# Kernel tuning notes

Hardware: AMD Instinct MI355X
Metric: run time of the kernel (lower is better)

The kernel has to match this reference:

```python
import jax, jax.numpy as jnp
import numpy as np

B, S, H, N = 2, 2048, 1024, 16
HN = H // N  # head dim = 64
EPS = 1e-12


def setup_inputs() -> dict:
    key = jax.random.key(0)
    ks = jax.random.split(key, 8)
    scale = 0.02
    return {
        "hidden_states": jax.random.normal(ks[0], (B, S, H), dtype=jnp.float32),
        "attention_mask": jnp.zeros((B, 1, 1, S), dtype=jnp.float32),
        "W_qkv": jax.random.normal(ks[1], (3 * H, H), dtype=jnp.float32) * scale,
        "b_qkv": jnp.zeros((3 * H,), dtype=jnp.float32),
        "W_out": jax.random.normal(ks[2], (H, H), dtype=jnp.float32) * scale,
        "b_out": jnp.zeros((H,), dtype=jnp.float32),
        "ln_gamma": jnp.ones((H,), dtype=jnp.float32),
        "ln_beta": jnp.zeros((H,), dtype=jnp.float32),
    }


def reference(hidden_states, attention_mask, W_qkv, b_qkv, W_out, b_out, ln_gamma, ln_beta):
    # QKV projection: torch Linear => x @ W.T + b
    qkv = jnp.einsum("bsh,oh->bso", hidden_states, W_qkv) + b_qkv  # [B,S,3H]
    q, k, v = jnp.split(qkv, 3, axis=-1)

    def heads(t):  # [B,S,H] -> [B,N,S,HN]
        return t.reshape(B, S, N, HN).transpose(0, 2, 1, 3)

    q, k, v = heads(q), heads(k), heads(v)
    nf = jnp.sqrt(jnp.sqrt(jnp.float32(HN)))
    scores = jnp.einsum("bnsd,bntd->bnst", q / nf, k / nf) + attention_mask  # [B,N,S,S]
    probs = jax.nn.softmax(scores, axis=-1)
    ctx = jnp.einsum("bnst,bntd->bnsd", probs, v)  # [B,N,S,HN]
    ctx = ctx.transpose(0, 2, 1, 3).reshape(B, S, H)

    # output dense + residual + LayerNorm
    out = jnp.einsum("bsh,oh->bso", ctx, W_out) + b_out
    x = out + hidden_states
    mean = jnp.mean(x, axis=-1, keepdims=True)
    var = jnp.mean(jnp.square(x - mean), axis=-1, keepdims=True)
    return (x - mean) * jax.lax.rsqrt(var + EPS) * ln_gamma + ln_beta
```

## Files before the change

kernel.cpp:

```cpp
#include <hip/hip_runtime.h>
#include <hip/hip_bf16.h>
#include <math.h>

#define Bq  2
#define Sq  2048
#define Hq  1024
#define Nq  16
#define HNq 64
#define Mq  (Bq*Sq)
#define H3q (3*Hq)

#define LOG2E 1.44269504088896340736f

typedef __attribute__((ext_vector_type(8))) short           short8;
typedef __attribute__((ext_vector_type(4))) short           short4s;
typedef __attribute__((ext_vector_type(8))) unsigned short  ushortx8;
typedef __attribute__((ext_vector_type(4))) unsigned short  ushortx4;
typedef __attribute__((ext_vector_type(4))) float           floatx4;

__device__ __forceinline__ unsigned short f2bf(float f) {
    union { float f; unsigned int u; } x; x.f = f;
    unsigned int r = (x.u + 0x7fffu + ((x.u >> 16) & 1u)) >> 16;
    return (unsigned short)r;
}

__device__ __forceinline__ unsigned int pkbf(float a, float b) {
    float2 t; t.x = a; t.y = b;
    __hip_bfloat162 h = __float22bfloat162_rn(t);
    union { __hip_bfloat162 h; unsigned int u; } c; c.h = h;
    return c.u;
}

__device__ __forceinline__ float bf2f(unsigned short v) {
    union { unsigned int u; float f; } x; x.u = (unsigned int)v << 16;
    return x.f;
}

__device__ __forceinline__ void gload16(const unsigned short* g, unsigned short* l) {
    __builtin_amdgcn_global_load_lds(
        (__attribute__((address_space(1))) void*)(unsigned long long)(g),
        (__attribute__((address_space(3))) void*)(unsigned int)(unsigned long long)(l),
        16, 0, 0);
}

__device__ __forceinline__ int swz(int r) { return (r ^ (r >> 2)) & 3; }

#define N_HID ((size_t)Mq * Hq)
#define N_HW  (N_HID + (size_t)H3q * Hq)
#define N_ALL (N_HW + (size_t)Hq * Hq)

__global__ __launch_bounds__(256) void cvt_all(
    const float* __restrict__ hidden, const float* __restrict__ wqkv,
    const float* __restrict__ wout, unsigned short* __restrict__ dst)
{
    size_t i = ((size_t)blockIdx.x * 256 + threadIdx.x) * 8;
    const float* src;
    if (i < N_HID)      src = hidden + i;
    else if (i < N_HW)  src = wqkv + (i - N_HID);
    else                src = wout + (i - N_HW);
    float4 a = *(const float4*)(src);
    float4 b = *(const float4*)(src + 4);
    union { unsigned int u[4]; ushortx8 s; } o;
    o.u[0] = pkbf(a.x, a.y); o.u[1] = pkbf(a.z, a.w);
    o.u[2] = pkbf(b.x, b.y); o.u[3] = pkbf(b.z, b.w);
    *(ushortx8*)(dst + i) = o.s;
}

__global__ __launch_bounds__(256) void cvt_mask(
    const float* __restrict__ mask, unsigned short* __restrict__ em2)
{
    const int t0   = (blockIdx.x * 256 + threadIdx.x) * 8;
    const int b    = t0 >> 11;
    const int t2   = t0 & 2047;
    const int kt   = t2 >> 6;
    const int t3   = t2 & 63;
    const int ks   = t3 >> 5;
    const int quad = (t3 >> 3) & 3;
    const int kb   = kt * 64 + ks * 32 + quad * 4;
    const float* mp = mask + (size_t)b * Sq + kb;
    float4 m0 = *(const float4*)(mp);
    float4 m1 = *(const float4*)(mp + 16);
    union { unsigned int u[4]; ushortx8 s; } o;
    o.u[0] = pkbf(exp2f(m0.x * LOG2E), exp2f(m0.y * LOG2E));
    o.u[1] = pkbf(exp2f(m0.z * LOG2E), exp2f(m0.w * LOG2E));
    o.u[2] = pkbf(exp2f(m1.x * LOG2E), exp2f(m1.y * LOG2E));
    o.u[3] = pkbf(exp2f(m1.z * LOG2E), exp2f(m1.w * LOG2E));
    *(ushortx8*)(em2 + t0) = o.s;
}

#define TM 128
#define TN 128
#define TK 32

__global__ __launch_bounds__(256) void gemm_mfma_qkv(
    const unsigned short* __restrict__ A, const unsigned short* __restrict__ Bw,
    const float* __restrict__ bias, const float* __restrict__ mask,
    unsigned short* __restrict__ Qb, unsigned short* __restrict__ Kd,
    unsigned short* __restrict__ V5, int K)
{
    __shared__ unsigned short As[2][TM][TK];
    __shared__ unsigned short Bs[2][TN][TK];

    const int tid = threadIdx.x;
    const int w = tid >> 6, lane = tid & 63;
    const int l15 = lane & 15, quad = lane >> 4;
    const int wr = (w & 1) * 64;
    const int wc = (w >> 1) * 64;
    const int row0 = blockIdx.y * TM;
    const int col0 = blockIdx.x * TN;

    const int srow16 = lane >> 2;
    const int sgd    = lane & 3;
    const int sgsrc  = (sgd ^ swz(srow16)) * 8;

    floatx4 acc[4][4];
    #pragma unroll
    for (int i = 0; i < 4; i++)
        #pragma unroll
        for (int j = 0; j < 4; j++) acc[i][j] = (floatx4){0.f,0.f,0.f,0.f};

    const int aswz = swz(l15) * 8;
    const int NK = K / TK;

    #pragma unroll
    for (int c = 0; c < 2; c++) {
        int seg = w * 2 + c;
        int r = seg * 16 + srow16;
        gload16(A  + (size_t)(row0 + r) * K + sgsrc, &As[0][seg * 16][0]);
        gload16(Bw + (size_t)(col0 + r) * K + sgsrc, &Bs[0][seg * 16][0]);
    }

    #pragma unroll 2
    for (int k = 0; k < NK; ++k) {
        asm volatile("s_waitcnt vmcnt(0)" ::: "memory");
        __builtin_amdgcn_s_barrier();
        __builtin_amdgcn_sched_barrier(0);

        const int cur = k & 1;
        if (k + 1 < NK) {
            const int k0n = (k + 1) * TK;
            #pragma unroll
            for (int c = 0; c < 2; c++) {
                int seg = w * 2 + c;
                int r = seg * 16 + srow16;
                gload16(A  + (size_t)(row0 + r) * K + k0n + sgsrc, &As[cur ^ 1][seg * 16][0]);
                gload16(Bw + (size_t)(col0 + r) * K + k0n + sgsrc, &Bs[cur ^ 1][seg * 16][0]);
            }
        }
        __builtin_amdgcn_sched_barrier(0);

        short8 af[4], bf[4];
        #pragma unroll
        for (int i = 0; i < 4; i++)
            af[i] = *(const short8*)&As[cur][wr + i * 16 + l15][(quad * 8) ^ aswz];
        #pragma unroll
        for (int j = 0; j < 4; j++)
            bf[j] = *(const short8*)&Bs[cur][wc + j * 16 + l15][(quad * 8) ^ aswz];
        __builtin_amdgcn_s_setprio(1);
        #pragma unroll
        for (int i = 0; i < 4; i++)
            #pragma unroll
            for (int j = 0; j < 4; j++)
                acc[i][j] = __builtin_amdgcn_mfma_f32_16x16x32_bf16(af[i], bf[j], acc[i][j], 0, 0, 0);
        __builtin_amdgcn_s_setprio(0);
    }

    const int cls = col0 >> 10;

    if (cls == 2) {
        #pragma unroll
        for (int i = 0; i < 4; i++) {
            const int rb = row0 + wr + i * 16 + quad * 4;
            const int b  = rb >> 11;
            const int s  = rb & (Sq - 1);
            const int kt32 = s >> 6;
            const int sw   = s & 63;
            const int kg   = sw >> 2;
            const int ks   = kg >> 3;
            const int q2   = kg & 3;
            const int hi   = (kg >> 2) & 1;
            float expm[4];
            #pragma unroll
            for (int rr = 0; rr < 4; rr++)
                expm[rr] = exp2f(mask[(size_t)b * Sq + s + rr] * LOG2E);
            #pragma unroll
            for (int j = 0; j < 4; j++) {
                const int c  = col0 + wc + j * 16 + l15;
                const int c2 = c - 2 * Hq;
                const int n  = c2 >> 6, d = c2 & 63;
                const int dt = d >> 4, dl = d & 15;
                const float bia = bias[c];
                ushortx4 o;
                #pragma unroll
                for (int rr = 0; rr < 4; rr++)
                    o[rr] = f2bf((acc[i][j][rr] + bia) * expm[rr]);
                const size_t off = (((size_t)(b * Nq + n) * 32 + kt32) << 12)
                                 + (size_t)((ks * 16 + dt * 4 + q2) * 128 + dl * 8 + hi * 4);
                *(ushortx4*)&V5[off] = o;
            }
        }
    } else {
        unsigned short* __restrict__ dst = (cls == 0) ? Qb : Kd;
        const int cshift = (cls == 0) ? 0 : Hq;
        const float qs = (cls == 0) ? (0.125f * LOG2E) : 1.0f;
        #pragma unroll
        for (int i = 0; i < 4; i++) {
            const int rb = row0 + wr + i * 16 + quad * 4;
            #pragma unroll
            for (int j = 0; j < 4; j++) {
                const int c = col0 + wc + j * 16 + l15;
                const float bia = bias[c];
                #pragma unroll
                for (int rr = 0; rr < 4; rr++)
                    dst[(size_t)(rb + rr) * Hq + (c - cshift)] =
                        f2bf((acc[i][j][rr] + bia) * qs);
            }
        }
    }
}

__global__ __launch_bounds__(256) void gemm_mfma_out(
    const unsigned short* __restrict__ A, const unsigned short* __restrict__ Bw,
    const float* __restrict__ bias, const float* __restrict__ res,
    unsigned short* __restrict__ X, int M, int Nd, int K)
{
    __shared__ unsigned short As[2][TM][TK];
    __shared__ unsigned short Bs[2][TN][TK];

    const int tid = threadIdx.x;
    const int w = tid >> 6, lane = tid & 63;
    const int l15 = lane & 15, quad = lane >> 4;
    const int wr = (w & 1) * 64;
    const int wc = (w >> 1) * 64;
    const int row0 = blockIdx.y * TM;
    const int col0 = blockIdx.x * TN;

    const int srow16 = lane >> 2;
    const int sgd    = lane & 3;
    const int sgsrc  = (sgd ^ swz(srow16)) * 8;

    floatx4 acc[4][4];
    #pragma unroll
    for (int i = 0; i < 4; i++)
        #pragma unroll
        for (int j = 0; j < 4; j++) acc[i][j] = (floatx4){0.f,0.f,0.f,0.f};

    const int aswz = swz(l15) * 8;
    const int NK = K / TK;

    #pragma unroll
    for (int c = 0; c < 2; c++) {
        int seg = w * 2 + c;
        int r = seg * 16 + srow16;
        gload16(A  + (size_t)(row0 + r) * K + sgsrc, &As[0][seg * 16][0]);
        gload16(Bw + (size_t)(col0 + r) * K + sgsrc, &Bs[0][seg * 16][0]);
    }

    #pragma unroll 2
    for (int k = 0; k < NK; ++k) {
        asm volatile("s_waitcnt vmcnt(0)" ::: "memory");
        __builtin_amdgcn_s_barrier();
        __builtin_amdgcn_sched_barrier(0);

        const int cur = k & 1;
        if (k + 1 < NK) {
            const int k0n = (k + 1) * TK;
            #pragma unroll
            for (int c = 0; c < 2; c++) {
                int seg = w * 2 + c;
                int r = seg * 16 + srow16;
                gload16(A  + (size_t)(row0 + r) * K + k0n + sgsrc, &As[cur ^ 1][seg * 16][0]);
                gload16(Bw + (size_t)(col0 + r) * K + k0n + sgsrc, &Bs[cur ^ 1][seg * 16][0]);
            }
        }
        __builtin_amdgcn_sched_barrier(0);

        short8 af[4], bf[4];
        #pragma unroll
        for (int i = 0; i < 4; i++)
            af[i] = *(const short8*)&As[cur][wr + i * 16 + l15][(quad * 8) ^ aswz];
        #pragma unroll
        for (int j = 0; j < 4; j++)
            bf[j] = *(const short8*)&Bs[cur][wc + j * 16 + l15][(quad * 8) ^ aswz];
        __builtin_amdgcn_s_setprio(1);
        #pragma unroll
        for (int i = 0; i < 4; i++)
            #pragma unroll
            for (int j = 0; j < 4; j++)
                acc[i][j] = __builtin_amdgcn_mfma_f32_16x16x32_bf16(af[i], bf[j], acc[i][j], 0, 0, 0);
        __builtin_amdgcn_s_setprio(0);
    }

    #pragma unroll
    for (int i = 0; i < 4; i++) {
        const int rb = row0 + wr + i * 16 + quad * 4;
        #pragma unroll
        for (int j = 0; j < 4; j++) {
            const int c = col0 + wc + j * 16 + l15;
            const float bia = bias[c];
            #pragma unroll
            for (int rr = 0; rr < 4; rr++) {
                X[(size_t)(rb + rr) * Nd + c] =
                    f2bf(acc[i][j][rr] + bia + res[(size_t)(rb + rr) * Nd + c]);
            }
        }
    }
}

#define KTILES 16

__device__ __forceinline__ floatx4 mfma16(short8 a, short8 b, floatx4 c) {
    return __builtin_amdgcn_mfma_f32_16x16x32_bf16(a, b, c, 0, 0, 0);
}

__device__ __forceinline__ void do_lpv(
    const short8 (&pf0)[2], const short8 (&pf1)[2], const short8 (&mf)[2],
    const short8 (&vf)[8],
    floatx4 (&oacc0)[4], floatx4 (&oacc1)[4],
    floatx4 &lacc0, floatx4 &lacc1)
{
    __builtin_amdgcn_s_setprio(1);
    lacc0 = mfma16(mf[0], pf0[0], lacc0);
    lacc0 = mfma16(mf[1], pf0[1], lacc0);
    lacc1 = mfma16(mf[0], pf1[0], lacc1);
    lacc1 = mfma16(mf[1], pf1[1], lacc1);
    #pragma unroll
    for (int dt = 0; dt < 4; dt++) {
        oacc0[dt] = mfma16(vf[dt],     pf0[0], oacc0[dt]);
        oacc1[dt] = mfma16(vf[dt],     pf1[0], oacc1[dt]);
        oacc0[dt] = mfma16(vf[4 + dt], pf0[1], oacc0[dt]);
        oacc1[dt] = mfma16(vf[4 + dt], pf1[1], oacc1[dt]);
    }
    __builtin_amdgcn_s_setprio(0);
}

template<bool HAVER, bool PREF, int VWAIT>
__device__ __forceinline__ void attn_body(
    int kt,
    unsigned short (&KsL)[2][64][64],
    const unsigned short* kp, size_t kstep,
    const unsigned short* Vb, const unsigned short* e2b,
    int w, int l15, int quad,
    const short8 (&qf0)[2], const short8 (&qf1)[2],
    short8 (&vf)[8],
    const short8 (&pfR0)[2], const short8 (&pfR1)[2], const short8 (&mfR)[2],
    short8 (&pfW0)[2], short8 (&pfW1)[2], short8 (&mfW)[2],
    floatx4 (&oacc0)[4], floatx4 (&oacc1)[4],
    floatx4 &lacc0, floatx4 &lacc1)
{
    asm volatile("s_waitcnt vmcnt(%0)" :: "i"(VWAIT) : "memory");
    __builtin_amdgcn_s_barrier();
    __builtin_amdgcn_sched_barrier(0);

    const int cur = kt & 1;
    if (PREF) {
        const unsigned short* kpn = kp + (size_t)(kt + 1) * kstep;
        gload16(kpn,                  &KsL[cur ^ 1][w * 16][0]);
        gload16(kpn + (size_t)8 * Hq, &KsL[cur ^ 1][w * 16 + 8][0]);
    }
    __builtin_amdgcn_sched_barrier(0);

    const unsigned short* ep = e2b + kt * 64;
    mfW[0] = *(const short8*)(ep + quad * 8);
    mfW[1] = *(const short8*)(ep + 32 + quad * 8);

    floatx4 s0[4], s1[4];
    #pragma unroll
    for (int ct = 0; ct < 4; ct++) {
        s0[ct] = (floatx4){0.f,0.f,0.f,0.f};
        s1[ct] = (floatx4){0.f,0.f,0.f,0.f};
    }
    __builtin_amdgcn_s_setprio(1);
    #pragma unroll
    for (int ks = 0; ks < 2; ks++) {
        #pragma unroll
        for (int ct = 0; ct < 4; ct++) {
            short8 af = *(const short8*)&KsL[cur][ct * 16 + l15][((4 * ks + quad) ^ (l15 & 7)) * 8];
            s0[ct] = mfma16(af, qf0[ks], s0[ct]);
            s1[ct] = mfma16(af, qf1[ks], s1[ct]);
        }
    }
    __builtin_amdgcn_s_setprio(0);

    #pragma unroll
    for (int ks = 0; ks < 2; ks++) {
        union { unsigned int u[4]; short8 s; } pk;
        #pragma unroll
        for (int h = 0; h < 2; h++) {
            const int ct = ks * 2 + h;
            pk.u[h * 2]     = pkbf(exp2f(s0[ct][0]), exp2f(s0[ct][1]));
            pk.u[h * 2 + 1] = pkbf(exp2f(s0[ct][2]), exp2f(s0[ct][3]));
        }
        pfW0[ks] = pk.s;
    }
    #pragma unroll
    for (int ks = 0; ks < 2; ks++) {
        union { unsigned int u[4]; short8 s; } pk;
        #pragma unroll
        for (int h = 0; h < 2; h++) {
            const int ct = ks * 2 + h;
            pk.u[h * 2]     = pkbf(exp2f(s1[ct][0]), exp2f(s1[ct][1]));
            pk.u[h * 2 + 1] = pkbf(exp2f(s1[ct][2]), exp2f(s1[ct][3]));
        }
        pfW1[ks] = pk.s;
    }

    if (HAVER)
        do_lpv(pfR0, pfR1, mfR, vf, oacc0, oacc1, lacc0, lacc1);

    const unsigned short* vt = Vb + (size_t)kt * 4096 + quad * 128 + l15 * 8;
    vf[0] = *(const short8*)(vt);
    vf[1] = *(const short8*)(vt + 512);
    vf[2] = *(const short8*)(vt + 1024);
    vf[3] = *(const short8*)(vt + 1536);
    vf[4] = *(const short8*)(vt + 2048);
    vf[5] = *(const short8*)(vt + 2560);
    vf[6] = *(const short8*)(vt + 3072);
    vf[7] = *(const short8*)(vt + 3584);
}

__global__ __launch_bounds__(256) void attn_mfma(
    const unsigned short* __restrict__ Qb, const unsigned short* __restrict__ Kd,
    const unsigned short* __restrict__ V5, const unsigned short* __restrict__ em2,
    unsigned short* __restrict__ Opart, float* __restrict__ Lpart)
{
    __shared__ unsigned short Ks[2][64][64];

    const int tid  = threadIdx.x;
    const int w    = tid >> 6;
    const int lane = tid & 63;
    const int l15  = lane & 15;
    const int quad = lane >> 4;

    const int qtile = blockIdx.x;
    const int bn    = blockIdx.y;
    const int z     = blockIdx.z;
    const int n     = bn & 15;
    const int b     = bn >> 4;

    const int kbase = z * (KTILES * 64);

    short8 qf0[2], qf1[2];
    {
        const int qrow0 = qtile * 128 + w * 16 + l15;
        const unsigned short* qp = Qb + (size_t)(b * Sq + qrow0) * Hq + n * HNq + quad * 8;
        qf0[0] = *(const short8*)(qp);
        qf0[1] = *(const short8*)(qp + 32);
        qp += (size_t)64 * Hq;
        qf1[0] = *(const short8*)(qp);
        qf1[1] = *(const short8*)(qp + 32);
    }

    floatx4 oacc0[4], oacc1[4];
    #pragma unroll
    for (int dt = 0; dt < 4; dt++) {
        oacc0[dt] = (floatx4){0.f,0.f,0.f,0.f};
        oacc1[dt] = (floatx4){0.f,0.f,0.f,0.f};
    }
    floatx4 lacc0 = (floatx4){0.f,0.f,0.f,0.f};
    floatx4 lacc1 = (floatx4){0.f,0.f,0.f,0.f};

    const int krow8 = lane >> 3;
    const int kgr   = (lane & 7) ^ (krow8 & 7);
    const unsigned short* kp = Kd + (size_t)(b * Sq + kbase + w * 16 + krow8) * Hq
                                  + n * HNq + kgr * 8;
    const size_t kstep = (size_t)64 * Hq;

    gload16(kp,                  &Ks[0][w * 16][0]);
    gload16(kp + (size_t)8 * Hq, &Ks[0][w * 16 + 8][0]);

    const unsigned short* Vb  = V5 + ((size_t)(b * Nq + n) * 32 + z * KTILES) * 4096;
    const unsigned short* e2b = em2 + (size_t)(b * 32 + z * KTILES) * 64;

    short8 vf[8];
    short8 pfA0[2], pfA1[2], mfA[2];
    short8 pfB0[2], pfB1[2], mfB[2];

    attn_body<false, true, 0>(0, Ks, kp, kstep, Vb, e2b, w, l15, quad,
        qf0, qf1, vf, pfB0, pfB1, mfB, pfA0, pfA1, mfA, oacc0, oacc1, lacc0, lacc1);

    #pragma unroll 1
    for (int kt = 1; kt < KTILES - 1; kt += 2) {
        attn_body<true, true, 10>(kt, Ks, kp, kstep, Vb, e2b, w, l15, quad,
            qf0, qf1, vf, pfA0, pfA1, mfA, pfB0, pfB1, mfB, oacc0, oacc1, lacc0, lacc1);
        attn_body<true, true, 10>(kt + 1, Ks, kp, kstep, Vb, e2b, w, l15, quad,
            qf0, qf1, vf, pfB0, pfB1, mfB, pfA0, pfA1, mfA, oacc0, oacc1, lacc0, lacc1);
    }
    attn_body<true, false, 10>(KTILES - 1, Ks, kp, kstep, Vb, e2b, w, l15, quad,
        qf0, qf1, vf, pfA0, pfA1, mfA, pfB0, pfB1, mfB, oacc0, oacc1, lacc0, lacc1);
    do_lpv(pfB0, pfB1, mfB, vf, oacc0, oacc1, lacc0, lacc1);

    unsigned short* Ow = Opart + (size_t)z * Mq * Hq;
    #pragma unroll
    for (int sub = 0; sub < 2; sub++) {
        const float l_i = sub ? lacc1[0] : lacc0[0];
        const int qrow = qtile * 128 + sub * 64 + w * 16 + l15;
        if (quad == 0)
            Lpart[(size_t)z * Mq * Nq + (size_t)(b * Sq + qrow) * Nq + n] = l_i;
        #pragma unroll
        for (int dt = 0; dt < 4; dt++) {
            const floatx4 oa = sub ? oacc1[dt] : oacc0[dt];
            union { unsigned int u[2]; ushortx4 s; } o;
            o.u[0] = pkbf(oa[0], oa[1]);
            o.u[1] = pkbf(oa[2], oa[3]);
            const int col = n * HNq + dt * 16 + quad * 4;
            *(ushortx4*)&Ow[(size_t)(b * Sq + qrow) * Hq + col] = o.s;
        }
    }
}

__global__ __launch_bounds__(256) void attn_merge(
    const unsigned short* __restrict__ Opart, const float* __restrict__ Lpart,
    unsigned short* __restrict__ ctx)
{
    const size_t idx = ((size_t)blockIdx.x * 256 + threadIdx.x) * 4;
    const int row = (int)(idx >> 10);
    const int n   = ((int)idx >> 6) & 15;
    const float l = Lpart[(size_t)row * Nq + n]
                  + Lpart[(size_t)Mq * Nq + (size_t)row * Nq + n];
    const float inv = 1.0f / l;
    ushortx4 a = *(const ushortx4*)(Opart + idx);
    ushortx4 c = *(const ushortx4*)(Opart + (size_t)Mq * Hq + idx);
    union { unsigned int u[2]; ushortx4 s; } o;
    o.u[0] = pkbf((bf2f(a[0]) + bf2f(c[0])) * inv, (bf2f(a[1]) + bf2f(c[1])) * inv);
    o.u[1] = pkbf((bf2f(a[2]) + bf2f(c[2])) * inv, (bf2f(a[3]) + bf2f(c[3])) * inv);
    *(ushortx4*)(ctx + idx) = o.s;
}

__global__ __launch_bounds__(256) void ln_kernel(
    const unsigned short* __restrict__ X, const float* __restrict__ gamma,
    const float* __restrict__ beta, float* __restrict__ out)
{
    const int row = blockIdx.x;
    const int c0  = threadIdx.x * 4;
    ushortx4 xv = *(const ushortx4*)(X + (size_t)row * Hq + c0);
    float vals[4];
    float lsum = 0.0f;
    #pragma unroll
    for (int i = 0; i < 4; i++) { vals[i] = bf2f(xv[i]); lsum += vals[i]; }

    __shared__ float red[8];
    const int wid = threadIdx.x >> 6, lane = threadIdx.x & 63;

    float s = lsum;
    #pragma unroll
    for (int off = 32; off >= 1; off >>= 1) s += __shfl_xor(s, off, 64);
    if (lane == 0) red[wid] = s;
    __syncthreads();
    const float mean = (red[0] + red[1] + red[2] + red[3]) * (1.0f / Hq);

    float v = 0.0f;
    #pragma unroll
    for (int i = 0; i < 4; i++) { float d = vals[i] - mean; v += d * d; }
    #pragma unroll
    for (int off = 32; off >= 1; off >>= 1) v += __shfl_xor(v, off, 64);
    if (lane == 0) red[4 + wid] = v;
    __syncthreads();
    const float var  = (red[4] + red[5] + red[6] + red[7]) * (1.0f / Hq);
    const float rstd = rsqrtf(var + 1e-12f);

    float4 gm = *(const float4*)(gamma + c0);
    float4 bt = *(const float4*)(beta + c0);
    float4 o;
    o.x = (vals[0] - mean) * rstd * gm.x + bt.x;
    o.y = (vals[1] - mean) * rstd * gm.y + bt.y;
    o.z = (vals[2] - mean) * rstd * gm.z + bt.z;
    o.w = (vals[3] - mean) * rstd * gm.w + bt.w;
    *(float4*)(out + (size_t)row * Hq + c0) = o;
}

extern "C" void kernel_launch(void* const* d_in, const int* in_sizes, int n_in,
                              void* d_out, int out_size, void* d_ws, size_t ws_size,
                              hipStream_t stream)
{
    const float* hidden = (const float*)d_in[0];
    const float* mask   = (const float*)d_in[1];
    const float* W_qkv  = (const float*)d_in[2];
    const float* b_qkv  = (const float*)d_in[3];
    const float* W_out  = (const float*)d_in[4];
    const float* b_out  = (const float*)d_in[5];
    const float* gamma  = (const float*)d_in[6];
    const float* beta   = (const float*)d_in[7];
    float* out = (float*)d_out;

    const size_t nHid  = (size_t)Mq * Hq;
    const size_t nWq   = (size_t)H3q * Hq;
    const size_t nWo   = (size_t)Hq * Hq;
    const size_t nCtx  = (size_t)Mq * Hq;

    unsigned short* hidden_bf = (unsigned short*)d_ws;
    unsigned short* Wqkv_bf   = hidden_bf + nHid;
    unsigned short* Wout_bf   = Wqkv_bf + nWq;
    unsigned short* qb        = Wout_bf + nWo;
    unsigned short* kd        = qb + nHid;
    unsigned short* v5        = kd + nHid;
    unsigned short* ctx_bf    = v5 + nHid;
    unsigned short* x_bf      = ctx_bf + nCtx;
    unsigned short* opart     = x_bf + nHid;
    float*          lpart     = (float*)(opart + 2 * nHid);
    unsigned short* em2       = (unsigned short*)(lpart + 2 * (size_t)Mq * Nq);

    dim3 blk(256);

    cvt_all<<<dim3((int)(N_ALL / 2048)), blk, 0, stream>>>(
        hidden, W_qkv, W_out, hidden_bf);
    cvt_mask<<<dim3(2), blk, 0, stream>>>(mask, em2);

    gemm_mfma_qkv<<<dim3(H3q / TN, Mq / TM), blk, 0, stream>>>(
        hidden_bf, Wqkv_bf, b_qkv, mask, qb, kd, v5, Hq);

    attn_mfma<<<dim3(Sq / 128, Bq * Nq, 2), blk, 0, stream>>>(
        qb, kd, v5, em2, opart, lpart);

    attn_merge<<<dim3((int)(nCtx / 1024)), blk, 0, stream>>>(
        opart, lpart, ctx_bf);

    gemm_mfma_out<<<dim3(Hq / TN, Mq / TM), blk, 0, stream>>>(
        ctx_bf, Wout_bf, b_out, hidden, x_bf, Mq, Hq, Hq);

    ln_kernel<<<dim3(Mq), blk, 0, stream>>>(x_bf, gamma, beta, out);
}
```

Before: 228.4 us.

## Triple-buffer GEMM k-loop with two-ahead prefetch and fuse mask conversion launch

Both the QKV and output projection GEMMs move from double to triple-buffered LDS tiles, prefetching two k-steps ahead and waiting with vmcnt(4) so that one stage of global loads stays in flight across the barrier. The separate mask-conversion kernel is folded into the bulk conversion kernel as two extra blocks, removing one launch. LDS use per block rises to 48KB, which may reduce occupancy. The loop unroll drops to 1, which adds modulo-3 index arithmetic.

```diff
diff --git a/kernel.cpp b/kernel.cpp
--- a/kernel.cpp
+++ b/kernel.cpp
@@ -48,12 +48,35 @@
 #define N_HID ((size_t)Mq * Hq)
 #define N_HW  (N_HID + (size_t)H3q * Hq)
 #define N_ALL (N_HW + (size_t)Hq * Hq)
+#define CVT_BLKS ((int)(N_ALL / 2048))
 
 __global__ __launch_bounds__(256) void cvt_all(
     const float* __restrict__ hidden, const float* __restrict__ wqkv,
-    const float* __restrict__ wout, unsigned short* __restrict__ dst)
-{
-    size_t i = ((size_t)blockIdx.x * 256 + threadIdx.x) * 8;
+    const float* __restrict__ wout, const float* __restrict__ mask,
+    unsigned short* __restrict__ dst, unsigned short* __restrict__ em2)
+{
+    const int bid = blockIdx.x;
+    if (bid >= CVT_BLKS) {
+        const int t0   = ((bid - CVT_BLKS) * 256 + threadIdx.x) * 8;
+        const int b    = t0 >> 11;
+        const int t2   = t0 & 2047;
+        const int kt   = t2 >> 6;
+        const int t3   = t2 & 63;
+        const int ks   = t3 >> 5;
+        const int quad = (t3 >> 3) & 3;
+        const int kb   = kt * 64 + ks * 32 + quad * 4;
+        const float* mp = mask + (size_t)b * Sq + kb;
+        float4 m0 = *(const float4*)(mp);
+        float4 m1 = *(const float4*)(mp + 16);
+        union { unsigned int u[4]; ushortx8 s; } o;
+        o.u[0] = pkbf(exp2f(m0.x * LOG2E), exp2f(m0.y * LOG2E));
+        o.u[1] = pkbf(exp2f(m0.z * LOG2E), exp2f(m0.w * LOG2E));
+        o.u[2] = pkbf(exp2f(m1.x * LOG2E), exp2f(m1.y * LOG2E));
+        o.u[3] = pkbf(exp2f(m1.z * LOG2E), exp2f(m1.w * LOG2E));
+        *(ushortx8*)(em2 + t0) = o.s;
+        return;
+    }
+    size_t i = ((size_t)bid * 256 + threadIdx.x) * 8;
     const float* src;
     if (i < N_HID)      src = hidden + i;
     else if (i < N_HW)  src = wqkv + (i - N_HID);
@@ -66,28 +89,6 @@
     *(ushortx8*)(dst + i) = o.s;
 }
 
-__global__ __launch_bounds__(256) void cvt_mask(
-    const float* __restrict__ mask, unsigned short* __restrict__ em2)
-{
-    const int t0   = (blockIdx.x * 256 + threadIdx.x) * 8;
-    const int b    = t0 >> 11;
-    const int t2   = t0 & 2047;
-    const int kt   = t2 >> 6;
-    const int t3   = t2 & 63;
-    const int ks   = t3 >> 5;
-    const int quad = (t3 >> 3) & 3;
-    const int kb   = kt * 64 + ks * 32 + quad * 4;
-    const float* mp = mask + (size_t)b * Sq + kb;
-    float4 m0 = *(const float4*)(mp);
-    float4 m1 = *(const float4*)(mp + 16);
-    union { unsigned int u[4]; ushortx8 s; } o;
-    o.u[0] = pkbf(exp2f(m0.x * LOG2E), exp2f(m0.y * LOG2E));
-    o.u[1] = pkbf(exp2f(m0.z * LOG2E), exp2f(m0.w * LOG2E));
-    o.u[2] = pkbf(exp2f(m1.x * LOG2E), exp2f(m1.y * LOG2E));
-    o.u[3] = pkbf(exp2f(m1.z * LOG2E), exp2f(m1.w * LOG2E));
-    *(ushortx8*)(em2 + t0) = o.s;
-}
-
 #define TM 128
 #define TN 128
 #define TK 32
@@ -98,8 +99,8 @@
     unsigned short* __restrict__ Qb, unsigned short* __restrict__ Kd,
     unsigned short* __restrict__ V5, int K)
 {
-    __shared__ unsigned short As[2][TM][TK];
-    __shared__ unsigned short Bs[2][TN][TK];
+    __shared__ unsigned short As[3][TM][TK];
+    __shared__ unsigned short Bs[3][TN][TK];
 
     const int tid = threadIdx.x;
     const int w = tid >> 6, lane = tid & 63;
@@ -123,28 +124,33 @@
     const int NK = K / TK;
 
     #pragma unroll
-    for (int c = 0; c < 2; c++) {
-        int seg = w * 2 + c;
-        int r = seg * 16 + srow16;
-        gload16(A  + (size_t)(row0 + r) * K + sgsrc, &As[0][seg * 16][0]);
-        gload16(Bw + (size_t)(col0 + r) * K + sgsrc, &Bs[0][seg * 16][0]);
-    }
-
-    #pragma unroll 2
+    for (int t = 0; t < 2; t++) {
+        #pragma unroll
+        for (int c = 0; c < 2; c++) {
+            int seg = w * 2 + c;
+            int r = seg * 16 + srow16;
+            gload16(A  + (size_t)(row0 + r) * K + t * TK + sgsrc, &As[t][seg * 16][0]);
+            gload16(Bw + (size_t)(col0 + r) * K + t * TK + sgsrc, &Bs[t][seg * 16][0]);
+        }
+    }
+
+    #pragma unroll 1
     for (int k = 0; k < NK; ++k) {
-        asm volatile("s_waitcnt vmcnt(0)" ::: "memory");
+        if (k + 1 < NK) asm volatile("s_waitcnt vmcnt(4)" ::: "memory");
+        else            asm volatile("s_waitcnt vmcnt(0)" ::: "memory");
         __builtin_amdgcn_s_barrier();
         __builtin_amdgcn_sched_barrier(0);
 
-        const int cur = k & 1;
-        if (k + 1 < NK) {
-            const int k0n = (k + 1) * TK;
+        const int cur = k % 3;
+        if (k + 2 < NK) {
+            const int nb  = (k + 2) % 3;
+            const int k0n = (k + 2) * TK;
             #pragma unroll
             for (int c = 0; c < 2; c++) {
                 int seg = w * 2 + c;
                 int r = seg * 16 + srow16;
-                gload16(A  + (size_t)(row0 + r) * K + k0n + sgsrc, &As[cur ^ 1][seg * 16][0]);
-                gload16(Bw + (size_t)(col0 + r) * K + k0n + sgsrc, &Bs[cur ^ 1][seg * 16][0]);
+                gload16(A  + (size_t)(row0 + r) * K + k0n + sgsrc, &As[nb][seg * 16][0]);
+                gload16(Bw + (size_t)(col0 + r) * K + k0n + sgsrc, &Bs[nb][seg * 16][0]);
             }
         }
         __builtin_amdgcn_sched_barrier(0);
@@ -224,8 +230,8 @@
     const float* __restrict__ bias, const float* __restrict__ res,
     unsigned short* __restrict__ X, int M, int Nd, int K)
 {
-    __shared__ unsigned short As[2][TM][TK];
-    __shared__ unsigned short Bs[2][TN][TK];
+    __shared__ unsigned short As[3][TM][TK];
+    __shared__ unsigned short Bs[3][TN][TK];
 
     const int tid = threadIdx.x;
     const int w = tid >> 6, lane = tid & 63;
@@ -249,28 +255,33 @@
     const int NK = K / TK;
 
     #pragma unroll
-    for (int c = 0; c < 2; c++) {
-        int seg = w * 2 + c;
-        int r = seg * 16 + srow16;
-        gload16(A  + (size_t)(row0 + r) * K + sgsrc, &As[0][seg * 16][0]);
-        gload16(Bw + (size_t)(col0 + r) * K + sgsrc, &Bs[0][seg * 16][0]);
-    }
-
-    #pragma unroll 2
+    for (int t = 0; t < 2; t++) {
+        #pragma unroll
+        for (int c = 0; c < 2; c++) {
+            int seg = w * 2 + c;
+            int r = seg * 16 + srow16;
+            gload16(A  + (size_t)(row0 + r) * K + t * TK + sgsrc, &As[t][seg * 16][0]);
+            gload16(Bw + (size_t)(col0 + r) * K + t * TK + sgsrc, &Bs[t][seg * 16][0]);
+        }
+    }
+
+    #pragma unroll 1
     for (int k = 0; k < NK; ++k) {
-        asm volatile("s_waitcnt vmcnt(0)" ::: "memory");
+        if (k + 1 < NK) asm volatile("s_waitcnt vmcnt(4)" ::: "memory");
+        else            asm volatile("s_waitcnt vmcnt(0)" ::: "memory");
         __builtin_amdgcn_s_barrier();
         __builtin_amdgcn_sched_barrier(0);
 
-        const int cur = k & 1;
-        if (k + 1 < NK) {
-            const int k0n = (k + 1) * TK;
+        const int cur = k % 3;
+        if (k + 2 < NK) {
+            const int nb  = (k + 2) % 3;
+            const int k0n = (k + 2) * TK;
             #pragma unroll
             for (int c = 0; c < 2; c++) {
                 int seg = w * 2 + c;
                 int r = seg * 16 + srow16;
-                gload16(A  + (size_t)(row0 + r) * K + k0n + sgsrc, &As[cur ^ 1][seg * 16][0]);
-                gload16(Bw + (size_t)(col0 + r) * K + k0n + sgsrc, &Bs[cur ^ 1][seg * 16][0]);
+                gload16(A  + (size_t)(row0 + r) * K + k0n + sgsrc, &As[nb][seg * 16][0]);
+                gload16(Bw + (size_t)(col0 + r) * K + k0n + sgsrc, &Bs[nb][seg * 16][0]);
             }
         }
         __builtin_amdgcn_sched_barrier(0);
@@ -602,9 +613,8 @@
 
     dim3 blk(256);
 
-    cvt_all<<<dim3((int)(N_ALL / 2048)), blk, 0, stream>>>(
-        hidden, W_qkv, W_out, hidden_bf);
-    cvt_mask<<<dim3(2), blk, 0, stream>>>(mask, em2);
+    cvt_all<<<dim3(CVT_BLKS + 2), blk, 0, stream>>>(
+        hidden, W_qkv, W_out, mask, hidden_bf, em2);
 
     gemm_mfma_qkv<<<dim3(H3q / TN, Mq / TM), blk, 0, stream>>>(
         hidden_bf, Wqkv_bf, b_qkv, mask, qb, kd, v5, Hq);
```

After: 218.8 us. -4.2%, faster.
